# Kernel tuning notes

Measured on AMD Instinct MI355X. Metric: run time of the kernel, lower is better.

## Reference

```python
import jax, jax.numpy as jnp
import numpy as np
from jax import lax

B, S, T = 256, 2048, 64


def setup_inputs() -> dict:
    key = jax.random.key(0)
    k1, k2, k3 = jax.random.split(key, 3)
    emissions = jax.random.normal(k1, (B, S, T), dtype=jnp.float32)
    tags = jax.random.randint(k2, (B, S), 0, T, dtype=jnp.int64)
    mask = jnp.ones((B, S), dtype=bool)
    # learned parameter: transitions ~ U(-0.1, 0.1) per reset_parameters
    transitions = jax.random.uniform(k3, (T, T), dtype=jnp.float32, minval=-0.1, maxval=0.1)
    return {"emissions": emissions, "transitions": transitions, "tags": tags, "mask": mask}


def _crf_nll(emissions, transitions, tags, mask):
    # emissions [B,S,T], tags [B,S] int, mask [B,S] bool -> scalar NLL
    em = jnp.swapaxes(emissions, 0, 1)        # [S,B,T]
    tg = jnp.swapaxes(tags, 0, 1)             # [S,B]
    mk = jnp.swapaxes(mask, 0, 1)             # [S,B]
    bsz = tg.shape[1]
    batch_range = jnp.arange(bsz)

    # ---- score(emissions, tags, mask): fully vectorized over seq ----
    em_at_tags = jnp.take_along_axis(em, tg[..., None], axis=-1)[..., 0]   # [S,B]
    trans_steps = transitions[tg[:-1], tg[1:]]                              # [S-1,B]
    step_scores = (trans_steps + em_at_tags[1:]) * mk[1:].astype(em.dtype)  # [S-1,B]
    gold_score = em[0, batch_range, tg[0]] + jnp.sum(step_scores, axis=0)   # [B]

    # ---- normalization: logsumexp semiring scan over seq ----
    def step(score, inp):
        e_t, m_t = inp                                   # [B,T], [B]
        # score[b, i] + transitions[i, j] + e_t[b, j] -> lse over i
        s_ = jax.nn.logsumexp(score[:, :, None] + transitions[None] + e_t[:, None, :], axis=1)
        score = jnp.where(m_t[:, None], s_, score)
        return score, None

    final, _ = lax.scan(step, em[0], (em[1:], mk[1:]))
    log_z = jax.nn.logsumexp(final, axis=-1)             # [B]

    return -jnp.mean(gold_score - log_z)


def reference(emissions, transitions, tags, mask):
    return _crf_nll(emissions, transitions, tags, mask)
```

## Files before the change

### kernel.cpp

```cpp
#include <hip/hip_runtime.h>
#include <cstdint>

#define BB 256
#define SS 2048
#define TT 64
#define LOG64 4.158883083359672

#define OUTB 0
#define GBASE 256
#define LBASE 512
#define LSIZE (256 * 16 * 64)
#define PBASE_F (LBASE + LSIZE)

#define M_SPLIT 1024
#define WS_STRIDE 144

typedef float  f32x16 __attribute__((ext_vector_type(16)));
typedef float  f32x4v __attribute__((ext_vector_type(4)));
typedef unsigned int u32x4 __attribute__((ext_vector_type(4)));
typedef int    i32x2v __attribute__((ext_vector_type(2)));
typedef __bf16 bf16x8 __attribute__((ext_vector_type(8)));

__device__ __forceinline__ int ldtag(const uint32_t* tw, int i, int is64) {
    return (int)tw[i << is64];
}

__device__ __forceinline__ unsigned cvt_pk_bf16(float lo, float hi) {
    unsigned r;
    asm("v_cvt_pk_bf16_f32 %0, %1, %2" : "=v"(r) : "v"(lo), "v"(hi));
    return r;
}

__device__ __forceinline__ f32x16 mfma32(u32x4 a, u32x4 b, f32x16 c) {
#if __has_builtin(__builtin_amdgcn_mfma_f32_32x32x16_bf16)
    return __builtin_amdgcn_mfma_f32_32x32x16_bf16(
        __builtin_bit_cast(bf16x8, a), __builtin_bit_cast(bf16x8, b), c, 0, 0, 0);
#else
    f32x16 d;
    asm volatile("v_mfma_f32_32x32x16_bf16 %0, %1, %2, %3\n\ts_nop 7\n\ts_nop 7"
        : "=v"(d) : "v"(a), "v"(b), "v"(c));
    return d;
#endif
}

__device__ __forceinline__ void plswap(unsigned& a, unsigned& b, bool hb) {
#if __has_builtin(__builtin_amdgcn_permlane32_swap)
    (void)hb;
    i32x2v r = __builtin_amdgcn_permlane32_swap((int)a, (int)b, false, false);
    a = (unsigned)r[0]; b = (unsigned)r[1];
#else
    const unsigned xa = __shfl_xor(a, 32);
    const unsigned xb = __shfl_xor(b, 32);
    const unsigned na = hb ? xb : a;
    const unsigned nb = hb ? b : xa;
    a = na; b = nb;
#endif
}

__global__ __launch_bounds__(256, 4) void crf_seg32_kernel(
    const float* __restrict__ em, const float* __restrict__ trans,
    float* __restrict__ ws, int sshift)
{
    const int tid = threadIdx.x;
    const int wv = tid >> 6;
    const int l  = tid & 63;
    const int c = l & 31, h = l >> 5;
    const bool hb = (h != 0);
    const int u  = blockIdx.x * 4 + wv;
    const int bs = u >> 1;
    const int w  = u & 1;
    const int b  = bs >> sshift;
    const int s  = bs & ((1 << sshift) - 1);
    const int cn = w * 32 + c;
    __shared__ __align__(16) float f_lds[4][TT];
    float* fl = f_lds[wv];

    const f32x16 ZZ = {0,0,0,0,0,0,0,0,0,0,0,0,0,0,0,0};

#define MKA(NM, mt, kt) u32x4 NM; { \
        const int kb = 16*(kt) + 8*h; const int mc = 32*(mt) + c; \
        const float e0 = __expf(trans[(kb+0)*64 + mc]) * 0.015625f; \
        const float e1 = __expf(trans[(kb+1)*64 + mc]) * 0.015625f; \
        const float e2 = __expf(trans[(kb+2)*64 + mc]) * 0.015625f; \
        const float e3 = __expf(trans[(kb+3)*64 + mc]) * 0.015625f; \
        const float e4 = __expf(trans[(kb+4)*64 + mc]) * 0.015625f; \
        const float e5 = __expf(trans[(kb+5)*64 + mc]) * 0.015625f; \
        const float e6 = __expf(trans[(kb+6)*64 + mc]) * 0.015625f; \
        const float e7 = __expf(trans[(kb+7)*64 + mc]) * 0.015625f; \
        NM[0] = cvt_pk_bf16(e0, e1); NM[1] = cvt_pk_bf16(e2, e3); \
        NM[2] = cvt_pk_bf16(e4, e5); NM[3] = cvt_pk_bf16(e6, e7); }
    MKA(A00, 0, 0) MKA(A01, 0, 1) MKA(A02, 0, 2) MKA(A03, 0, 3)
    MKA(A10, 1, 0) MKA(A11, 1, 1) MKA(A12, 1, 2) MKA(A13, 1, 3)
#undef MKA

#define MKB(NM, kt) u32x4 NM; { \
        const int kb = 16*(kt) + 8*h; \
        NM[0] = cvt_pk_bf16(kb+0==cn?1.f:0.f, kb+1==cn?1.f:0.f); \
        NM[1] = cvt_pk_bf16(kb+2==cn?1.f:0.f, kb+3==cn?1.f:0.f); \
        NM[2] = cvt_pk_bf16(kb+4==cn?1.f:0.f, kb+5==cn?1.f:0.f); \
        NM[3] = cvt_pk_bf16(kb+6==cn?1.f:0.f, kb+7==cn?1.f:0.f); }
    MKB(B0, 0) MKB(B1, 1) MKB(B2, 2) MKB(B3, 3)
#undef MKB

    const size_t ebase = (size_t)b * (SS * TT);
    const int nseg = 1 << sshift;
    const int L  = SS >> sshift;
    const int t0 = s * L + 1;
    const int t1 = (s == nseg - 1) ? (SS - 1) : (s + 1) * L;
    const int nst = t1 - t0 + 1;

    float p0 = em[ebase + (size_t)(t0 + 0) * TT + l];
    float p1 = em[ebase + (size_t)(t0 + 1) * TT + l];
    float p2 = em[ebase + (size_t)(t0 + 2) * TT + l];
    float p3 = em[ebase + (size_t)(t0 + 3) * TT + l];

    float logacc = 0.f;
    f32x16 c0, c1;

    for (int si = 0; si < nst; ++si) {
        const float fr = __expf(p0);
        p0 = p1; p1 = p2; p2 = p3;
        int tp = t0 + si + 4; if (tp > SS - 1) tp = SS - 1;
        p3 = em[ebase + (size_t)tp * TT + l];

        fl[l] = fr;

        c0 = mfma32(A00, B0, ZZ);  c1 = mfma32(A10, B0, ZZ);
        c0 = mfma32(A01, B1, c0);  c1 = mfma32(A11, B1, c1);
        c0 = mfma32(A02, B2, c0);  c1 = mfma32(A12, B2, c1);
        c0 = mfma32(A03, B3, c0);  c1 = mfma32(A13, B3, c1);

        const f32x4v f0 = *(const f32x4v*)(fl +  0 + 4*h);
        const f32x4v f1 = *(const f32x4v*)(fl +  8 + 4*h);
        const f32x4v f2 = *(const f32x4v*)(fl + 16 + 4*h);
        const f32x4v f3 = *(const f32x4v*)(fl + 24 + 4*h);
        const f32x4v f4 = *(const f32x4v*)(fl + 32 + 4*h);
        const f32x4v f5 = *(const f32x4v*)(fl + 40 + 4*h);
        const f32x4v f6 = *(const f32x4v*)(fl + 48 + 4*h);
        const f32x4v f7 = *(const f32x4v*)(fl + 56 + 4*h);
#define SC(C_, q, FV) { C_[4*(q)+0] *= FV[0]; C_[4*(q)+1] *= FV[1]; \
                        C_[4*(q)+2] *= FV[2]; C_[4*(q)+3] *= FV[3]; }
        SC(c0,0,f0) SC(c0,1,f1) SC(c0,2,f2) SC(c0,3,f3)
        SC(c1,0,f4) SC(c1,1,f5) SC(c1,2,f6) SC(c1,3,f7)
#undef SC

        if ((si & 7) == 7) {
            float mx = c0[0];
#define MX(v) mx = fmaxf(mx, v);
            MX(c0[1]) MX(c0[2]) MX(c0[3]) MX(c0[4]) MX(c0[5]) MX(c0[6]) MX(c0[7])
            MX(c0[8]) MX(c0[9]) MX(c0[10]) MX(c0[11]) MX(c0[12]) MX(c0[13]) MX(c0[14]) MX(c0[15])
            MX(c1[0]) MX(c1[1]) MX(c1[2]) MX(c1[3]) MX(c1[4]) MX(c1[5]) MX(c1[6]) MX(c1[7])
            MX(c1[8]) MX(c1[9]) MX(c1[10]) MX(c1[11]) MX(c1[12]) MX(c1[13]) MX(c1[14]) MX(c1[15])
#undef MX
            mx = fmaxf(mx, __shfl_xor(mx, 32));
            const float inv = __builtin_amdgcn_rcpf(mx);
            c0 *= inv; c1 *= inv;
            logacc += __logf(mx);
        }

#define FEED(Bd, C_, o) { \
        unsigned T0 = cvt_pk_bf16(C_[(o)+0], C_[(o)+1]); \
        unsigned T1 = cvt_pk_bf16(C_[(o)+2], C_[(o)+3]); \
        unsigned T2 = cvt_pk_bf16(C_[(o)+4], C_[(o)+5]); \
        unsigned T3 = cvt_pk_bf16(C_[(o)+6], C_[(o)+7]); \
        plswap(T0, T2, hb); plswap(T1, T3, hb); \
        Bd[0] = T0; Bd[1] = T1; Bd[2] = T2; Bd[3] = T3; }
        FEED(B0, c0, 0) FEED(B1, c0, 8) FEED(B2, c1, 0) FEED(B3, c1, 8)
#undef FEED
    }

    uint16_t* ptu = (uint16_t*)(ws + PBASE_F)
                  + (size_t)bs * 4096 + (size_t)cn * 64;
#define STQ(C_, q, base) { \
        *(unsigned*)(ptu + (base) + 8*(q) + 4*h)     = cvt_pk_bf16(C_[4*(q)+0], C_[4*(q)+1]); \
        *(unsigned*)(ptu + (base) + 8*(q) + 4*h + 2) = cvt_pk_bf16(C_[4*(q)+2], C_[4*(q)+3]); }
    STQ(c0,0,0) STQ(c0,1,0) STQ(c0,2,0) STQ(c0,3,0)
    STQ(c1,0,32) STQ(c1,1,32) STQ(c1,2,32) STQ(c1,3,32)
#undef STQ
    if (h == 0)
        ws[LBASE + bs * 64 + cn] = logacc + (float)((double)nst * LOG64);
}

__global__ __launch_bounds__(64) void crf_combine2(
    const float* __restrict__ em, float* __restrict__ ws, int sshift)
{
    const int b = blockIdx.x, m = threadIdx.x;
    const int nseg = 1 << sshift;
    __shared__ float xs[TT];
    float alpha = __expf(em[(size_t)b * (SS * TT) + m]);
    float logA = 0.f;
    for (int s = 0; s < nseg; ++s) {
        const int seg = b * nseg + s;
        const float Li = ws[LBASE + seg * 64 + m];
        float Lmax = Li;
        for (int off = 1; off < 64; off <<= 1) Lmax = fmaxf(Lmax, __shfl_xor(Lmax, off));
        xs[m] = alpha * __expf(Li - Lmax);
        const uint16_t* Pp = (const uint16_t*)(ws + PBASE_F) + (size_t)seg * 4096;
        float y = 0.f;
#pragma unroll 8
        for (int i = 0; i < TT; ++i) {
            const float pv = __uint_as_float((unsigned)Pp[i * 64 + m] << 16);
            y = fmaf(pv, xs[i], y);
        }
        logA += Lmax;
        float mx = y;
        for (int off = 1; off < 64; off <<= 1) mx = fmaxf(mx, __shfl_xor(mx, off));
        alpha = y * __builtin_amdgcn_rcpf(mx);
        logA += __logf(mx);
    }
    float ssum = alpha;
    for (int off = 1; off < 64; off <<= 1) ssum += __shfl_xor(ssum, off);
    if (m == 0)
        ws[OUTB + b] = ws[GBASE + b] - (logA + __logf(ssum));
}

__global__ __launch_bounds__(256) void crf_gold_kernel(
    const float* __restrict__ em, const float* __restrict__ trans,
    const uint32_t* __restrict__ tw, float* __restrict__ gdst, int gstride)
{
    const int b = blockIdx.x, tid = threadIdx.x;
    uint32_t orv = 0;
    for (int k = 1; k < 32; k += 2) orv |= tw[k];
    const int is64 = (orv == 0) ? 1 : 0;
    const int    tbase = b * SS;
    const size_t ebase = (size_t)b * SS * TT;
    float s = 0.0f;
    for (int t = tid; t < SS; t += 256) {
        const int tg = ldtag(tw, tbase + t, is64);
        float v = em[ebase + (size_t)t * TT + tg];
        if (t > 0) {
            const int tp = ldtag(tw, tbase + t - 1, is64);
            v += trans[tp * TT + tg];
        }
        s += v;
    }
    for (int off = 1; off < 64; off <<= 1) s += __shfl_xor(s, off);
    __shared__ float sh[4];
    if ((tid & 63) == 0) sh[tid >> 6] = s;
    __syncthreads();
    if (tid == 0) gdst[b * gstride] = sh[0] + sh[1] + sh[2] + sh[3];
}

__device__ __forceinline__ float qsum4(float v) {
    int a = __builtin_amdgcn_mov_dpp(__float_as_int(v), 0xB1, 0xF, 0xF, true);
    float v1 = v + __int_as_float(a);
    int b2 = __builtin_amdgcn_mov_dpp(__float_as_int(v1), 0x4E, 0xF, 0xF, true);
    return v1 + __int_as_float(b2);
}
#define LDS_BARRIER() asm volatile("s_waitcnt lgkmcnt(0)\n\ts_barrier" ::: "memory")

template <int DIR>
__device__ __forceinline__ void fb_run(const float* __restrict__ em,
                                       const float* __restrict__ trans,
                                       float* __restrict__ ws,
                                       float* __restrict__ qbuf,
                                       int b, int tid)
{
    const int l   = tid & 63;
    const int w   = tid >> 6;
    const int j   = (w << 4) | (l >> 2);
    const int sub = l & 3;
#define TRIDX(k) (DIR ? (j * 64 + (sub * 16 + (k))) : ((sub * 16 + (k)) * 64 + j))
#define ED(k) const float E##k = __expf(trans[TRIDX(k)]) * 0.015625f;
    ED(0) ED(1) ED(2) ED(3) ED(4) ED(5) ED(6) ED(7)
    ED(8) ED(9) ED(10) ED(11) ED(12) ED(13) ED(14) ED(15)
#undef ED
#undef TRIDX
    const size_t ebase  = (size_t)b * SS * TT;
    constexpr int nsteps = DIR ? (SS - M_SPLIT) : (M_SPLIT - 1);
    constexpr int estep  = DIR ? -TT : TT;
    constexpr int t0     = DIR ? (SS - 2) : 1;
    const float* ep = em + ebase + (size_t)t0 * TT + j;
    float p0 = ep[0];
    float p1 = ep[1 * estep];
    float p2 = ep[2 * estep];
    float p3 = ep[3 * estep];
    if (tid < TT) {
        const size_t it = DIR ? ((size_t)(SS - 1) * TT) : 0;
        qbuf[tid] = __expf(em[ebase + it + tid]);
    }
    LDS_BARRIER();
    float logsum = 0.0f;
    int cur = 0;
    for (int si = 0; si < nsteps; ++si) {
        const float e = p0;
        p0 = p1; p1 = p2; p2 = p3;
        p3 = ep[4 * estep];
        ep += estep;
        float* rb = qbuf + (cur << 6);
        float* wb = qbuf + ((cur ^ 1) << 6);
        const float4 q0 = *(const float4*)(rb + sub * 16 + 0);
        const float4 q1 = *(const float4*)(rb + sub * 16 + 4);
        const float4 q2 = *(const float4*)(rb + sub * 16 + 8);
        const float4 q3 = *(const float4*)(rb + sub * 16 + 12);
        float a0 = 0, a1 = 0, a2 = 0, a3 = 0;
        a0 = fmaf(q0.x, E0,  a0); a1 = fmaf(q0.y, E1,  a1);
        a2 = fmaf(q0.z, E2,  a2); a3 = fmaf(q0.w, E3,  a3);
        a0 = fmaf(q1.x, E4,  a0); a1 = fmaf(q1.y, E5,  a1);
        a2 = fmaf(q1.z, E6,  a2); a3 = fmaf(q1.w, E7,  a3);
        a0 = fmaf(q2.x, E8,  a0); a1 = fmaf(q2.y, E9,  a1);
        a2 = fmaf(q2.z, E10, a2); a3 = fmaf(q2.w, E11, a3);
        a0 = fmaf(q3.x, E12, a0); a1 = fmaf(q3.y, E13, a1);
        a2 = fmaf(q3.z, E14, a2); a3 = fmaf(q3.w, E15, a3);
        float dot = (a0 + a1) + (a2 + a3);
        dot = qsum4(dot);
        float fv = __expf(e);
        if (DIR && si == nsteps - 1) fv = 1.0f;
        float wval = dot * fv;
        if ((si & 63) == 63) {
            const float m = rb[0];
            wval *= __builtin_amdgcn_rcpf(m);
            if (tid == 0) logsum += __logf(m);
        }
        if (sub == 0) wb[j] = wval;
        LDS_BARRIER();
        cur ^= 1;
    }
    const float* fin = qbuf + (cur << 6);
    float* wsb = ws + (size_t)b * WS_STRIDE;
    if (tid < TT) wsb[(DIR ? TT : 0) + tid] = fin[tid];
    if (tid == 0) wsb[DIR ? 129 : 128] = (float)((double)nsteps * LOG64) + logsum;
}

__global__ __launch_bounds__(256) void crf_fb_kernel(
    const float* __restrict__ em, const float* __restrict__ trans,
    float* __restrict__ ws)
{
    const int b   = blockIdx.x & (BB - 1);
    const int dir = blockIdx.x >> 8;
    __shared__ __align__(16) float qbuf[2 * TT];
    if (dir == 0) fb_run<0>(em, trans, ws, qbuf, b, threadIdx.x);
    else          fb_run<1>(em, trans, ws, qbuf, b, threadIdx.x);
}

__global__ __launch_bounds__(64) void crf_combine_kernel(
    const float* __restrict__ ws, float* __restrict__ outb)
{
    const int b = blockIdx.x, lane = threadIdx.x;
    const float* wsb = ws + (size_t)b * WS_STRIDE;
    float p = wsb[lane] * wsb[64 + lane];
    for (int off = 1; off < 64; off <<= 1) p += __shfl_xor(p, off);
    if (lane == 0) {
        const float logz = wsb[128] + wsb[129] + __logf(p);
        outb[b] = wsb[130] - logz;
    }
}

__global__ __launch_bounds__(256) void crf_final_kernel(
    const float* __restrict__ vals, float* __restrict__ out)
{
    const int l = threadIdx.x;
    float v = vals[l];
    for (int off = 1; off < 64; off <<= 1) v += __shfl_xor(v, off);
    __shared__ float sh[4];
    if ((l & 63) == 0) sh[l >> 6] = v;
    __syncthreads();
    if (l == 0) out[0] = -(sh[0] + sh[1] + sh[2] + sh[3]) * (1.0f / BB);
}

extern "C" void kernel_launch(void* const* d_in, const int* in_sizes, int n_in,
                              void* d_out, int out_size, void* d_ws, size_t ws_size,
                              hipStream_t stream) {
    const float*    em    = (const float*)d_in[0];
    const float*    trans = (const float*)d_in[1];
    const uint32_t* tw    = (const uint32_t*)d_in[2];
    float* ws = (float*)d_ws;

    int sshift = 0;
    const size_t hdr = (size_t)PBASE_F * 4;
    if      (ws_size >= hdr + (((size_t)BB << 4) * 4096 * 2)) sshift = 4;
    else if (ws_size >= hdr + (((size_t)BB << 3) * 4096 * 2)) sshift = 3;
    else if (ws_size >= hdr + (((size_t)BB << 2) * 4096 * 2)) sshift = 2;
    else if (ws_size >= hdr + (((size_t)BB << 1) * 4096 * 2)) sshift = 1;

    if (sshift) {
        const int nwaves = (BB << sshift) * 2;
        crf_seg32_kernel<<<nwaves / 4, 256, 0, stream>>>(em, trans, ws, sshift);
        crf_gold_kernel<<<BB, 256, 0, stream>>>(em, trans, tw, ws + GBASE, 1);
        crf_combine2<<<BB, 64, 0, stream>>>(em, ws, sshift);
        crf_final_kernel<<<1, 256, 0, stream>>>(ws + OUTB, (float*)d_out);
        return;
    }

    float* outb = ws + (size_t)BB * WS_STRIDE;
    crf_fb_kernel<<<2 * BB, 256, 0, stream>>>(em, trans, ws);
    crf_gold_kernel<<<BB, 256, 0, stream>>>(em, trans, tw, ws + 130, WS_STRIDE);
    crf_combine_kernel<<<BB, 64, 0, stream>>>(ws, outb);
    crf_final_kernel<<<1, 256, 0, stream>>>(outb, (float*)d_out);
}
```

Baseline: 293.1 us.

## Fold gold-score blocks into segment kernel and double-buffer emission exp in LDS

The gold-path score computation now runs as extra blocks appended to the segment-scan kernel launch, which drops one kernel launch and lets that work overlap with the scan. Inside the scan loop the exp of the next emission row is written into a second LDS buffer one step ahead, and emission prefetch depth goes from 4 to 8 rows. The loop is unrolled by 8 with the renormalisation fixed to the last step of each group, so the per-step branch disappears. In exchange the kernel uses more registers and LDS, and the gold blocks share a launch whose LDS and occupancy are sized for the scan work.

```diff
diff --git a/kernel.cpp b/kernel.cpp
--- a/kernel.cpp
+++ b/kernel.cpp
@@ -57,11 +57,45 @@
 #endif
 }
 
+__device__ __forceinline__ void gold_body(
+    const float* __restrict__ em, const float* __restrict__ trans,
+    const uint32_t* __restrict__ tw, float* __restrict__ gdst, int gstride,
+    int b, int tid)
+{
+    uint32_t orv = 0;
+    for (int k = 1; k < 32; k += 2) orv |= tw[k];
+    const int is64 = (orv == 0) ? 1 : 0;
+    const int    tbase = b * SS;
+    const size_t ebase = (size_t)b * SS * TT;
+    float s = 0.0f;
+    for (int t = tid; t < SS; t += 256) {
+        const int tg = ldtag(tw, tbase + t, is64);
+        float v = em[ebase + (size_t)t * TT + tg];
+        if (t > 0) {
+            const int tp = ldtag(tw, tbase + t - 1, is64);
+            v += trans[tp * TT + tg];
+        }
+        s += v;
+    }
+    for (int off = 1; off < 64; off <<= 1) s += __shfl_xor(s, off);
+    __shared__ float sh[4];
+    if ((tid & 63) == 0) sh[tid >> 6] = s;
+    __syncthreads();
+    if (tid == 0) gdst[b * gstride] = sh[0] + sh[1] + sh[2] + sh[3];
+}
+
 __global__ __launch_bounds__(256, 4) void crf_seg32_kernel(
     const float* __restrict__ em, const float* __restrict__ trans,
-    float* __restrict__ ws, int sshift)
+    const uint32_t* __restrict__ tw,
+    float* __restrict__ ws, int sshift, int nsb)
 {
     const int tid = threadIdx.x;
+
+    if ((int)blockIdx.x >= nsb) {
+        gold_body(em, trans, tw, ws + GBASE, 1, (int)blockIdx.x - nsb, tid);
+        return;
+    }
+
     const int wv = tid >> 6;
     const int l  = tid & 63;
     const int c = l & 31, h = l >> 5;
@@ -72,8 +106,8 @@
     const int b  = bs >> sshift;
     const int s  = bs & ((1 << sshift) - 1);
     const int cn = w * 32 + c;
-    __shared__ __align__(16) float f_lds[4][TT];
-    float* fl = f_lds[wv];
+    __shared__ __align__(16) float f_lds[4][2][TT];
+    float* fl = &f_lds[wv][0][0];
 
     const f32x16 ZZ = {0,0,0,0,0,0,0,0,0,0,0,0,0,0,0,0};
 
@@ -113,51 +147,55 @@
     float p1 = em[ebase + (size_t)(t0 + 1) * TT + l];
     float p2 = em[ebase + (size_t)(t0 + 2) * TT + l];
     float p3 = em[ebase + (size_t)(t0 + 3) * TT + l];
+    float p4 = em[ebase + (size_t)(t0 + 4) * TT + l];
+    float p5 = em[ebase + (size_t)(t0 + 5) * TT + l];
+    float p6 = em[ebase + (size_t)(t0 + 6) * TT + l];
+    float p7 = em[ebase + (size_t)(t0 + 7) * TT + l];
 
     float logacc = 0.f;
     f32x16 c0, c1;
-
-    for (int si = 0; si < nst; ++si) {
-        const float fr = __expf(p0);
-        p0 = p1; p1 = p2; p2 = p3;
-        int tp = t0 + si + 4; if (tp > SS - 1) tp = SS - 1;
-        p3 = em[ebase + (size_t)tp * TT + l];
-
-        fl[l] = fr;
-
-        c0 = mfma32(A00, B0, ZZ);  c1 = mfma32(A10, B0, ZZ);
-        c0 = mfma32(A01, B1, c0);  c1 = mfma32(A11, B1, c1);
-        c0 = mfma32(A02, B2, c0);  c1 = mfma32(A12, B2, c1);
-        c0 = mfma32(A03, B3, c0);  c1 = mfma32(A13, B3, c1);
-
-        const f32x4v f0 = *(const f32x4v*)(fl +  0 + 4*h);
-        const f32x4v f1 = *(const f32x4v*)(fl +  8 + 4*h);
-        const f32x4v f2 = *(const f32x4v*)(fl + 16 + 4*h);
-        const f32x4v f3 = *(const f32x4v*)(fl + 24 + 4*h);
-        const f32x4v f4 = *(const f32x4v*)(fl + 32 + 4*h);
-        const f32x4v f5 = *(const f32x4v*)(fl + 40 + 4*h);
-        const f32x4v f6 = *(const f32x4v*)(fl + 48 + 4*h);
-        const f32x4v f7 = *(const f32x4v*)(fl + 56 + 4*h);
+    int si = 0;
+
+    fl[0 * TT + l] = __expf(p0);
+
+#define STEPB(KPAR, DOREN) { \
+        const float frn = __expf(p1); \
+        fl[(((KPAR)+1)&1) * TT + l] = frn;      \
+        p0=p1; p1=p2; p2=p3; p3=p4; p4=p5; p5=p6; p6=p7; \
+        { int tp = t0 + si + 8; if (tp > SS-1) tp = SS-1; \
+          p7 = em[ebase + (size_t)tp * TT + l]; } \
+        c0 = mfma32(A00, B0, ZZ);  c1 = mfma32(A10, B0, ZZ); \
+        c0 = mfma32(A01, B1, c0);  c1 = mfma32(A11, B1, c1); \
+        c0 = mfma32(A02, B2, c0);  c1 = mfma32(A12, B2, c1); \
+        c0 = mfma32(A03, B3, c0);  c1 = mfma32(A13, B3, c1); \
+        const float* flr = fl + ((KPAR)&1) * TT; \
+        const f32x4v f0 = *(const f32x4v*)(flr +  0 + 4*h); \
+        const f32x4v f1 = *(const f32x4v*)(flr +  8 + 4*h); \
+        const f32x4v f2 = *(const f32x4v*)(flr + 16 + 4*h); \
+        const f32x4v f3 = *(const f32x4v*)(flr + 24 + 4*h); \
+        const f32x4v f4 = *(const f32x4v*)(flr + 32 + 4*h); \
+        const f32x4v f5 = *(const f32x4v*)(flr + 40 + 4*h); \
+        const f32x4v f6 = *(const f32x4v*)(flr + 48 + 4*h); \
+        const f32x4v f7 = *(const f32x4v*)(flr + 56 + 4*h); \
+        SC(c0,0,f0) SC(c0,1,f1) SC(c0,2,f2) SC(c0,3,f3) \
+        SC(c1,0,f4) SC(c1,1,f5) SC(c1,2,f6) SC(c1,3,f7) \
+        if (DOREN) { \
+            float mx = c0[0]; \
+            MX(c0[1]) MX(c0[2]) MX(c0[3]) MX(c0[4]) MX(c0[5]) MX(c0[6]) MX(c0[7]) \
+            MX(c0[8]) MX(c0[9]) MX(c0[10]) MX(c0[11]) MX(c0[12]) MX(c0[13]) MX(c0[14]) MX(c0[15]) \
+            MX(c1[0]) MX(c1[1]) MX(c1[2]) MX(c1[3]) MX(c1[4]) MX(c1[5]) MX(c1[6]) MX(c1[7]) \
+            MX(c1[8]) MX(c1[9]) MX(c1[10]) MX(c1[11]) MX(c1[12]) MX(c1[13]) MX(c1[14]) MX(c1[15]) \
+            mx = fmaxf(mx, __shfl_xor(mx, 32)); \
+            const float inv = __builtin_amdgcn_rcpf(mx); \
+            c0 *= inv; c1 *= inv; \
+            logacc += __logf(mx); \
+        } \
+        FEED(B0, c0, 0) FEED(B1, c0, 8) FEED(B2, c1, 0) FEED(B3, c1, 8) \
+        ++si; }
+
 #define SC(C_, q, FV) { C_[4*(q)+0] *= FV[0]; C_[4*(q)+1] *= FV[1]; \
                         C_[4*(q)+2] *= FV[2]; C_[4*(q)+3] *= FV[3]; }
-        SC(c0,0,f0) SC(c0,1,f1) SC(c0,2,f2) SC(c0,3,f3)
-        SC(c1,0,f4) SC(c1,1,f5) SC(c1,2,f6) SC(c1,3,f7)
-#undef SC
-
-        if ((si & 7) == 7) {
-            float mx = c0[0];
 #define MX(v) mx = fmaxf(mx, v);
-            MX(c0[1]) MX(c0[2]) MX(c0[3]) MX(c0[4]) MX(c0[5]) MX(c0[6]) MX(c0[7])
-            MX(c0[8]) MX(c0[9]) MX(c0[10]) MX(c0[11]) MX(c0[12]) MX(c0[13]) MX(c0[14]) MX(c0[15])
-            MX(c1[0]) MX(c1[1]) MX(c1[2]) MX(c1[3]) MX(c1[4]) MX(c1[5]) MX(c1[6]) MX(c1[7])
-            MX(c1[8]) MX(c1[9]) MX(c1[10]) MX(c1[11]) MX(c1[12]) MX(c1[13]) MX(c1[14]) MX(c1[15])
-#undef MX
-            mx = fmaxf(mx, __shfl_xor(mx, 32));
-            const float inv = __builtin_amdgcn_rcpf(mx);
-            c0 *= inv; c1 *= inv;
-            logacc += __logf(mx);
-        }
-
 #define FEED(Bd, C_, o) { \
         unsigned T0 = cvt_pk_bf16(C_[(o)+0], C_[(o)+1]); \
         unsigned T1 = cvt_pk_bf16(C_[(o)+2], C_[(o)+3]); \
@@ -165,9 +203,20 @@
         unsigned T3 = cvt_pk_bf16(C_[(o)+6], C_[(o)+7]); \
         plswap(T0, T2, hb); plswap(T1, T3, hb); \
         Bd[0] = T0; Bd[1] = T1; Bd[2] = T2; Bd[3] = T3; }
-        FEED(B0, c0, 0) FEED(B1, c0, 8) FEED(B2, c1, 0) FEED(B3, c1, 8)
+
+    const int nouter = nst >> 3;
+    for (int o = 0; o < nouter; ++o) {
+        STEPB(0, false) STEPB(1, false) STEPB(0, false) STEPB(1, false)
+        STEPB(0, false) STEPB(1, false) STEPB(0, false) STEPB(1, true)
+    }
+    for (; si < nst; ) {
+        const int kp = si & 1;
+        if (kp == 0) { STEPB(0, false) } else { STEPB(1, false) }
+    }
 #undef FEED
-    }
+#undef MX
+#undef SC
+#undef STEPB
 
     uint16_t* ptu = (uint16_t*)(ws + PBASE_F)
                   + (size_t)bs * 4096 + (size_t)cn * 64;
@@ -218,27 +267,7 @@
     const float* __restrict__ em, const float* __restrict__ trans,
     const uint32_t* __restrict__ tw, float* __restrict__ gdst, int gstride)
 {
-    const int b = blockIdx.x, tid = threadIdx.x;
-    uint32_t orv = 0;
-    for (int k = 1; k < 32; k += 2) orv |= tw[k];
-    const int is64 = (orv == 0) ? 1 : 0;
-    const int    tbase = b * SS;
-    const size_t ebase = (size_t)b * SS * TT;
-    float s = 0.0f;
-    for (int t = tid; t < SS; t += 256) {
-        const int tg = ldtag(tw, tbase + t, is64);
-        float v = em[ebase + (size_t)t * TT + tg];
-        if (t > 0) {
-            const int tp = ldtag(tw, tbase + t - 1, is64);
-            v += trans[tp * TT + tg];
-        }
-        s += v;
-    }
-    for (int off = 1; off < 64; off <<= 1) s += __shfl_xor(s, off);
-    __shared__ float sh[4];
-    if ((tid & 63) == 0) sh[tid >> 6] = s;
-    __syncthreads();
-    if (tid == 0) gdst[b * gstride] = sh[0] + sh[1] + sh[2] + sh[3];
+    gold_body(em, trans, tw, gdst, gstride, blockIdx.x, threadIdx.x);
 }
 
 __device__ __forceinline__ float qsum4(float v) {
@@ -375,8 +404,8 @@
 
     if (sshift) {
         const int nwaves = (BB << sshift) * 2;
-        crf_seg32_kernel<<<nwaves / 4, 256, 0, stream>>>(em, trans, ws, sshift);
-        crf_gold_kernel<<<BB, 256, 0, stream>>>(em, trans, tw, ws + GBASE, 1);
+        const int nsb = nwaves / 4;
+        crf_seg32_kernel<<<nsb + BB, 256, 0, stream>>>(em, trans, tw, ws, sshift, nsb);
         crf_combine2<<<BB, 64, 0, stream>>>(em, ws, sshift);
         crf_final_kernel<<<1, 256, 0, stream>>>(ws + OUTB, (float*)d_out);
         return;
```

Result: faster. 272.0 us (-7.2%).
